# Optimization experiments

Measured on AMD Instinct MI355X. Metric: run time of the kernel, lower is better.

Reference implementation:

```python
import jax, jax.numpy as jnp
from jax import lax
import numpy as np

B, S, T = 512, 1024, 64  # batch, seq_len, tag_vocab_size


def setup_inputs() -> dict:
    key = jax.random.key(0)
    k1, k2, k3, k4 = jax.random.split(key, 4)
    tags = jax.random.randint(k1, (B, S), 0, T)
    # sequences sorted by length descending, as the original slicing scheme assumes
    lengths = jnp.sort(jax.random.randint(k2, (B,), 1, S + 1))[::-1]
    mask = jnp.arange(S)[None, :] < lengths[:, None]  # [B,S] bool
    emit_score = jax.random.normal(k3, (B, S, T), dtype=jnp.float32)
    transition = jax.random.normal(k4, (T, T), dtype=jnp.float32)
    return {"tags": tags, "mask": mask, "emit_score": emit_score, "transition": transition}


def reference(tags, mask, emit_score, transition):
    maskf = mask.astype(emit_score.dtype)
    # gold-path score: emission at gold tags + transition between consecutive gold tags
    score = jnp.take_along_axis(emit_score, tags[:, :, None], axis=2)[..., 0]  # [B,S]
    score = score.at[:, 1:].add(transition[tags[:, :-1], tags[:, 1:]])
    total_score = (score * maskf).sum(axis=1)  # [B]

    # forward algorithm (logsumexp-semiring scan over time)
    def step(d, inputs):
        emit_i, mask_i = inputs  # [B,T], [B]
        # log_sum[b, t_prev, t_cur] = d[b,t_prev] + transition[t_prev,t_cur] + emit_i[b,t_cur]
        cand = jax.nn.logsumexp(d[:, :, None] + transition[None, :, :] + emit_i[:, None, :], axis=1)
        d = jnp.where(mask_i[:, None], cand, d)  # finished sequences keep their alpha
        return d, None

    d0 = emit_score[:, 0]  # [B,T]
    emits_t = jnp.swapaxes(emit_score, 0, 1)[1:]  # [S-1,B,T]
    masks_t = mask.T[1:]  # [S-1,B]
    d, _ = lax.scan(step, d0, (emits_t, masks_t))
    log_z = jax.nn.logsumexp(d, axis=1)  # [B]
    return -(total_score - log_z)
```

## Files before the change

kernel.cpp:

```cpp
#include <hip/hip_runtime.h>
#include <stdint.h>

#define NB 512
#define SL 1024
#define NT 64

typedef float v4f __attribute__((ext_vector_type(4)));

__device__ __forceinline__ float wave_max6(float v) {
    #pragma unroll
    for (int off = 32; off >= 1; off >>= 1)
        v = fmaxf(v, __shfl_xor(v, off, 64));
    return v;
}
__device__ __forceinline__ float wave_sum_f(float v) {
    #pragma unroll
    for (int off = 32; off >= 1; off >>= 1)
        v += __shfl_xor(v, off, 64);
    return v;
}

__device__ __forceinline__ uint32_t bf16_rne(float x) {
    uint32_t u = __float_as_uint(x);
    return (u + 0x7fffu + ((u >> 16) & 1u)) >> 16;
}

__device__ __forceinline__ void dot2bf(float& acc, uint32_t a, uint32_t b) {
    asm("v_dot2_f32_bf16 %0, %1, %2, %0" : "+v"(acc) : "v"(a), "v"(b));
}

__global__ void __launch_bounds__(64) crf_fused_kernel(
    const int* __restrict__ tags, const void* __restrict__ mask,
    const float* __restrict__ emit, const float* __restrict__ trans,
    float* __restrict__ out)
{
    const int b = blockIdx.x;
    const int lane = threadIdx.x;
    const float* erow = emit + (size_t)b * SL * NT;
    const int* trow = tags + b * SL;

    const unsigned char* mb = (const unsigned char*)mask;
    const bool mask_is_i32 = ((mb[1] | mb[2] | mb[3]) == 0);

    float acc = 0.f; int cnt = 0;
    #pragma unroll
    for (int j = 0; j < 16; ++j) {
        const int i = lane + 64 * j;
        const int mk = mask_is_i32 ? (((const int*)mask)[(size_t)b * SL + i] != 0)
                                   : (mb[(size_t)b * SL + i] != 0);
        if (mk) {
            const int tg = trow[i];
            float val = erow[(size_t)i * NT + tg];
            if (i > 0) val += trans[trow[i - 1] * NT + tg];
            acc += val; cnt += 1;
        }
    }
    #pragma unroll
    for (int off = 32; off >= 1; off >>= 1) {
        acc += __shfl_xor(acc, off, 64);
        cnt += __shfl_xor(cnt, off, 64);
    }
    const float ts = acc;
    const int len = cnt;

    uint32_t Epk[NT / 2];
    #pragma unroll
    for (int m = 0; m < NT / 2; ++m) {
        uint32_t lo = bf16_rne(__expf(trans[(2 * m + 0) * NT + lane]));
        uint32_t hi = bf16_rne(__expf(trans[(2 * m + 1) * NT + lane]));
        Epk[m] = lo | (hi << 16);
    }

    __shared__ __align__(16) uint16_t vbuf16[NT];

    float d0 = erow[lane];
    float m0 = wave_max6(d0);
    float v = __expf(d0 - m0);
    float logacc = m0;

#define STEP(EX)                                                           \
    {                                                                      \
        vbuf16[lane] = (uint16_t)bf16_rne(v);                              \
        __builtin_amdgcn_wave_barrier();                                   \
        float a0 = 0.f, a1 = 0.f, a2 = 0.f, a3 = 0.f;                      \
        float a4 = 0.f, a5 = 0.f, a6 = 0.f, a7 = 0.f;                      \
        const uint4* vb = (const uint4*)vbuf16;                            \
        _Pragma("unroll")                                                  \
        for (int r = 0; r < 8; r += 2) {                                   \
            uint4 q0 = vb[r];                                              \
            uint4 q1 = vb[r + 1];                                          \
            dot2bf(a0, q0.x, Epk[4 * r + 0]);                              \
            dot2bf(a1, q0.y, Epk[4 * r + 1]);                              \
            dot2bf(a2, q0.z, Epk[4 * r + 2]);                              \
            dot2bf(a3, q0.w, Epk[4 * r + 3]);                              \
            dot2bf(a4, q1.x, Epk[4 * r + 4]);                              \
            dot2bf(a5, q1.y, Epk[4 * r + 5]);                              \
            dot2bf(a6, q1.z, Epk[4 * r + 6]);                              \
            dot2bf(a7, q1.w, Epk[4 * r + 7]);                              \
        }                                                                  \
        float h = ((a0 + a1) + (a2 + a3)) + ((a4 + a5) + (a6 + a7));       \
        v = h * (EX);                                                      \
    }

    const int nstep = len - 1;
    const int ngrp = nstep >> 2;
    int i = 1;

    v4f emq;
    if (ngrp > 0) {
        emq.x = erow[(i + 0) * NT + lane];
        emq.y = erow[(i + 1) * NT + lane];
        emq.z = erow[(i + 2) * NT + lane];
        emq.w = erow[(i + 3) * NT + lane];
    }
    for (int g = 0; g < ngrp; ++g) {
        float ex0 = __expf(emq.x), ex1 = __expf(emq.y);
        float ex2 = __expf(emq.z), ex3 = __expf(emq.w);
        const int ip = i + 4;
        if (g + 1 < ngrp) {
            emq.x = erow[(ip + 0) * NT + lane];
            emq.y = erow[(ip + 1) * NT + lane];
            emq.z = erow[(ip + 2) * NT + lane];
            emq.w = erow[(ip + 3) * NT + lane];
        }
        STEP(ex0)
        STEP(ex1)
        STEP(ex2)
        STEP(ex3)
        {
            uint32_t sb = __builtin_amdgcn_readfirstlane(__float_as_uint(v));
            int ex = (int)((sb >> 23) & 0xffu);
            v *= __uint_as_float((uint32_t)(254 - ex) << 23);
            logacc += (float)(ex - 127) * 0.69314718055994530942f;
        }
        i += 4;
    }
    for (; i < len; ++i) {
        float e = __expf(erow[i * NT + lane]);
        STEP(e)
    }
#undef STEP

    float sum = wave_sum_f(v);
    float log_z = logacc + __logf(sum);
    if (lane == 0) out[b] = -(ts - log_z);
}

extern "C" void kernel_launch(void* const* d_in, const int* in_sizes, int n_in,
                              void* d_out, int out_size, void* d_ws, size_t ws_size,
                              hipStream_t stream) {
    (void)in_sizes; (void)n_in; (void)out_size; (void)d_ws; (void)ws_size;
    const int*   tags  = (const int*)d_in[0];
    const void*  mask  = d_in[1];
    const float* emit  = (const float*)d_in[2];
    const float* trans = (const float*)d_in[3];
    float* out = (float*)d_out;

    crf_fused_kernel<<<dim3(NB), dim3(64), 0, stream>>>(tags, mask, emit, trans, out);
}
```

Measured before the change: 385.8 us.

## Batch 16 sequences per wave with MFMA scan over precomputed bf16 exp-emissions

```diff
diff --git a/kernel.cpp b/kernel.cpp
--- a/kernel.cpp
+++ b/kernel.cpp
@@ -4,32 +4,222 @@
 #define NB 512
 #define SL 1024
 #define NT 64
-
-typedef float v4f __attribute__((ext_vector_type(4)));
-
-__device__ __forceinline__ float wave_max6(float v) {
-    #pragma unroll
-    for (int off = 32; off >= 1; off >>= 1)
-        v = fmaxf(v, __shfl_xor(v, off, 64));
-    return v;
-}
-__device__ __forceinline__ float wave_sum_f(float v) {
-    #pragma unroll
-    for (int off = 32; off >= 1; off >>= 1)
-        v += __shfl_xor(v, off, 64);
-    return v;
-}
+#define NG 32
+#define GR 16
+
+typedef float f32x4 __attribute__((ext_vector_type(4)));
+typedef float v2f  __attribute__((ext_vector_type(2)));
+typedef short s16x8 __attribute__((ext_vector_type(8)));
 
 __device__ __forceinline__ uint32_t bf16_rne(float x) {
     uint32_t u = __float_as_uint(x);
     return (u + 0x7fffu + ((u >> 16) & 1u)) >> 16;
 }
+__device__ __forceinline__ uint32_t pack_bf16_trunc(float lo, float hi) {
+    return __builtin_amdgcn_perm(__float_as_uint(hi), __float_as_uint(lo), 0x07060302u);
+}
+__device__ __forceinline__ int t_of(int c, int q, int e) {
+    return 16 * (((c << 1) | (e >> 2))) + 4 * q + (e & 3);
+}
+
+__device__ __forceinline__ float wave_max6(float v) {
+    #pragma unroll
+    for (int off = 32; off >= 1; off >>= 1) v = fmaxf(v, __shfl_xor(v, off, 64));
+    return v;
+}
+__device__ __forceinline__ float wave_sum_f(float v) {
+    #pragma unroll
+    for (int off = 32; off >= 1; off >>= 1) v += __shfl_xor(v, off, 64);
+    return v;
+}
+
+__global__ void __launch_bounds__(256) exp_permute_kernel(
+    const float* __restrict__ emit, uint32_t* __restrict__ em4)
+{
+    __shared__ float tile[GR][16 * NT];
+    const int g = blockIdx.x >> 6;
+    const int i0 = (blockIdx.x & 63) << 4;
+    const int tid = threadIdx.x;
+
+    #pragma unroll 4
+    for (int bb = 0; bb < GR; ++bb) {
+        const float4* src = (const float4*)(emit + ((size_t)(GR * g + bb) * SL + i0) * NT);
+        ((float4*)tile[bb])[tid] = src[tid];
+    }
+    __syncthreads();
+
+    const int i_loc = tid >> 4;
+    const int lane0 = (tid & 15) << 2;
+    uint4 outq[8];
+    uint32_t* ov = (uint32_t*)outq;
+    #pragma unroll
+    for (int li = 0; li < 4; ++li) {
+        const int lane = lane0 + li, q = lane >> 4, r = lane & 15;
+        #pragma unroll
+        for (int d = 0; d < 8; ++d) {
+            const int c = d >> 2, dd = d & 3;
+            const int t0 = t_of(c, q, 2 * dd + 0);
+            const int t1 = t_of(c, q, 2 * dd + 1);
+            const float f0 = __expf(tile[r][i_loc * NT + t0]);
+            const float f1 = __expf(tile[r][i_loc * NT + t1]);
+            ov[li * 8 + d] = bf16_rne(f0) | (bf16_rne(f1) << 16);
+        }
+    }
+    uint4* dst = (uint4*)(em4 + (((size_t)(g * SL + i0 + i_loc) * 64) + lane0) * 8);
+    #pragma unroll
+    for (int k = 0; k < 8; ++k) dst[k] = outq[k];
+}
+
+template<bool DOREN>
+__device__ __forceinline__ void scan_step(
+    const s16x8 (&A)[4][2], uint4& B0, uint4& B1,
+    uint4 em0, uint4 em1, int i, int len, float& logacc)
+{
+    union U { uint4 u; s16x8 h; };
+    U b0; b0.u = B0; U b1; b1.u = B1;
+    const f32x4 z = {0.f, 0.f, 0.f, 0.f};
+    f32x4 acc[4];
+    #pragma unroll
+    for (int mi = 0; mi < 4; ++mi) {
+        f32x4 t = __builtin_amdgcn_mfma_f32_16x16x32_bf16(A[mi][0], b0.h, z, 0, 0, 0);
+        acc[mi]  = __builtin_amdgcn_mfma_f32_16x16x32_bf16(A[mi][1], b1.h, t, 0, 0, 0);
+    }
+    const uint32_t ed[8] = {em0.x, em0.y, em0.z, em0.w, em1.x, em1.y, em1.z, em1.w};
+    v2f p[8];
+    #pragma unroll
+    for (int s = 0; s < 8; ++s) {
+        const int c = s >> 2, d = s & 3;
+        const int mi = (c << 1) | (d >> 1);
+        const int rb = (d & 1) * 2;
+        const float elo = __uint_as_float(ed[s] << 16);
+        const float ehi = __uint_as_float(ed[s] & 0xffff0000u);
+        p[s].x = acc[mi][rb] * elo;
+        p[s].y = acc[mi][rb + 1] * ehi;
+    }
+    const bool alive = (i < len);
+    if (DOREN) {
+        float mx = 0.f;
+        #pragma unroll
+        for (int s = 0; s < 8; ++s) mx = fmaxf(mx, fmaxf(p[s].x, p[s].y));
+        mx = fmaxf(mx, __shfl_xor(mx, 16, 64));
+        mx = fmaxf(mx, __shfl_xor(mx, 32, 64));
+        const int ex = (int)((__float_as_uint(mx) >> 23) & 0xffu);
+        float sc = __uint_as_float((uint32_t)(254 - ex) << 23);
+        sc = alive ? sc : 1.0f;
+        logacc += alive ? (float)(ex - 127) * 0.69314718055994530942f : 0.0f;
+        #pragma unroll
+        for (int s = 0; s < 8; ++s) { p[s].x *= sc; p[s].y *= sc; }
+    }
+    uint32_t nd[8];
+    #pragma unroll
+    for (int s = 0; s < 8; ++s) nd[s] = pack_bf16_trunc(p[s].x, p[s].y);
+    B0.x = alive ? nd[0] : B0.x;  B0.y = alive ? nd[1] : B0.y;
+    B0.z = alive ? nd[2] : B0.z;  B0.w = alive ? nd[3] : B0.w;
+    B1.x = alive ? nd[4] : B1.x;  B1.y = alive ? nd[5] : B1.y;
+    B1.z = alive ? nd[6] : B1.z;  B1.w = alive ? nd[7] : B1.w;
+}
+
+__global__ void __launch_bounds__(64) crf_scan16_kernel(
+    const int* __restrict__ tags, const void* __restrict__ mask,
+    const float* __restrict__ emit, const float* __restrict__ trans,
+    const uint32_t* __restrict__ em4, float* __restrict__ out)
+{
+    const int g = blockIdx.x;
+    const int lane = threadIdx.x;
+    const int q = lane >> 4, r = lane & 15;
+    const int b = GR * g + r;
+
+    const unsigned char* mb = (const unsigned char*)mask;
+    const bool mask_is_i32 = ((mb[1] | mb[2] | mb[3]) == 0);
+    const int* trow = tags + (size_t)b * SL;
+    float acc = 0.f; int cnt = 0;
+    for (int ii = 0; ii < 256; ++ii) {
+        const int i = q * 256 + ii;
+        const int mk = mask_is_i32 ? (((const int*)mask)[(size_t)b * SL + i] != 0)
+                                   : (mb[(size_t)b * SL + i] != 0);
+        if (mk) {
+            const int tg = trow[i];
+            float val = emit[((size_t)b * SL + i) * NT + tg];
+            if (i > 0) val += trans[trow[i - 1] * NT + tg];
+            acc += val; cnt += 1;
+        }
+    }
+    acc += __shfl_xor(acc, 16, 64); acc += __shfl_xor(acc, 32, 64);
+    cnt += __shfl_xor(cnt, 16, 64); cnt += __shfl_xor(cnt, 32, 64);
+    const float ts = acc;
+    const int len = cnt;
+    int mx = len;
+    #pragma unroll
+    for (int off = 1; off <= 8; off <<= 1) mx = max(mx, __shfl_xor(mx, off, 64));
+    const int nstep = __builtin_amdgcn_readfirstlane(mx) - 1;
+
+    s16x8 A[4][2];
+    #pragma unroll
+    for (int mi = 0; mi < 4; ++mi)
+        #pragma unroll
+        for (int c = 0; c < 2; ++c)
+            #pragma unroll
+            for (int e = 0; e < 8; ++e) {
+                const int p = t_of(c, q, e);
+                A[mi][c][e] = (short)bf16_rne(__expf(trans[p * NT + (16 * mi + r)]));
+            }
+
+    const uint4* em_base = (const uint4*)em4 + (size_t)g * SL * 128 + (size_t)lane * 2;
+    uint4 B0 = em_base[0], B1 = em_base[1];
+    float logacc = 0.f;
+
+    int i = 1;
+    uint4 bufA[4][2], bufB[4][2];
+    #pragma unroll
+    for (int s = 0; s < 4; ++s) {
+        int sa = min(i + s, SL - 1), sb = min(i + 4 + s, SL - 1);
+        const uint4* pA = em_base + (size_t)sa * 128;
+        const uint4* pB = em_base + (size_t)sb * 128;
+        bufA[s][0] = pA[0]; bufA[s][1] = pA[1];
+        bufB[s][0] = pB[0]; bufB[s][1] = pB[1];
+    }
+    const int nsuper = nstep >> 3;
+    for (int sb = 0; sb < nsuper; ++sb) {
+        scan_step<false>(A, B0, B1, bufA[0][0], bufA[0][1], i + 0, len, logacc);
+        scan_step<false>(A, B0, B1, bufA[1][0], bufA[1][1], i + 1, len, logacc);
+        scan_step<false>(A, B0, B1, bufA[2][0], bufA[2][1], i + 2, len, logacc);
+        scan_step<true >(A, B0, B1, bufA[3][0], bufA[3][1], i + 3, len, logacc);
+        #pragma unroll
+        for (int s = 0; s < 4; ++s) {
+            const uint4* pp = em_base + (size_t)min(i + 8 + s, SL - 1) * 128;
+            bufA[s][0] = pp[0]; bufA[s][1] = pp[1];
+        }
+        scan_step<false>(A, B0, B1, bufB[0][0], bufB[0][1], i + 4, len, logacc);
+        scan_step<false>(A, B0, B1, bufB[1][0], bufB[1][1], i + 5, len, logacc);
+        scan_step<false>(A, B0, B1, bufB[2][0], bufB[2][1], i + 6, len, logacc);
+        scan_step<true >(A, B0, B1, bufB[3][0], bufB[3][1], i + 7, len, logacc);
+        #pragma unroll
+        for (int s = 0; s < 4; ++s) {
+            const uint4* pp = em_base + (size_t)min(i + 12 + s, SL - 1) * 128;
+            bufB[s][0] = pp[0]; bufB[s][1] = pp[1];
+        }
+        i += 8;
+    }
+    for (; i <= nstep; ++i) {
+        const uint4* pp = em_base + (size_t)i * 128;
+        scan_step<true>(A, B0, B1, pp[0], pp[1], i, len, logacc);
+    }
+
+    const uint32_t fd[8] = {B0.x, B0.y, B0.z, B0.w, B1.x, B1.y, B1.z, B1.w};
+    float sum = 0.f;
+    #pragma unroll
+    for (int s = 0; s < 8; ++s)
+        sum += __uint_as_float(fd[s] << 16) + __uint_as_float(fd[s] & 0xffff0000u);
+    sum += __shfl_xor(sum, 16, 64);
+    sum += __shfl_xor(sum, 32, 64);
+    const float log_z = logacc + __logf(sum);
+    if (lane < GR) out[(size_t)g * GR + lane] = -(ts - log_z);
+}
 
 __device__ __forceinline__ void dot2bf(float& acc, uint32_t a, uint32_t b) {
     asm("v_dot2_f32_bf16 %0, %1, %2, %0" : "+v"(acc) : "v"(a), "v"(b));
 }
-
-__global__ void __launch_bounds__(64) crf_fused_kernel(
+__global__ void __launch_bounds__(64) crf_fallback_kernel(
     const int* __restrict__ tags, const void* __restrict__ mask,
     const float* __restrict__ emit, const float* __restrict__ trans,
     float* __restrict__ out)
@@ -37,11 +227,9 @@
     const int b = blockIdx.x;
     const int lane = threadIdx.x;
     const float* erow = emit + (size_t)b * SL * NT;
-    const int* trow = tags + b * SL;
-
+    const int* trow = tags + (size_t)b * SL;
     const unsigned char* mb = (const unsigned char*)mask;
     const bool mask_is_i32 = ((mb[1] | mb[2] | mb[3]) == 0);
-
     float acc = 0.f; int cnt = 0;
     #pragma unroll
     for (int j = 0; j < 16; ++j) {
@@ -60,9 +248,7 @@
         acc += __shfl_xor(acc, off, 64);
         cnt += __shfl_xor(cnt, off, 64);
     }
-    const float ts = acc;
-    const int len = cnt;
-
+    const float ts = acc; const int len = cnt;
     uint32_t Epk[NT / 2];
     #pragma unroll
     for (int m = 0; m < NT / 2; ++m) {
@@ -70,77 +256,53 @@
         uint32_t hi = bf16_rne(__expf(trans[(2 * m + 1) * NT + lane]));
         Epk[m] = lo | (hi << 16);
     }
-
     __shared__ __align__(16) uint16_t vbuf16[NT];
-
     float d0 = erow[lane];
     float m0 = wave_max6(d0);
     float v = __expf(d0 - m0);
     float logacc = m0;
-
-#define STEP(EX)                                                           \
+#define FSTEP(EX)                                                          \
     {                                                                      \
         vbuf16[lane] = (uint16_t)bf16_rne(v);                              \
         __builtin_amdgcn_wave_barrier();                                   \
-        float a0 = 0.f, a1 = 0.f, a2 = 0.f, a3 = 0.f;                      \
-        float a4 = 0.f, a5 = 0.f, a6 = 0.f, a7 = 0.f;                      \
+        float a0=0.f,a1=0.f,a2=0.f,a3=0.f,a4=0.f,a5=0.f,a6=0.f,a7=0.f;     \
         const uint4* vb = (const uint4*)vbuf16;                            \
         _Pragma("unroll")                                                  \
-        for (int r = 0; r < 8; r += 2) {                                   \
-            uint4 q0 = vb[r];                                              \
-            uint4 q1 = vb[r + 1];                                          \
-            dot2bf(a0, q0.x, Epk[4 * r + 0]);                              \
-            dot2bf(a1, q0.y, Epk[4 * r + 1]);                              \
-            dot2bf(a2, q0.z, Epk[4 * r + 2]);                              \
-            dot2bf(a3, q0.w, Epk[4 * r + 3]);                              \
-            dot2bf(a4, q1.x, Epk[4 * r + 4]);                              \
-            dot2bf(a5, q1.y, Epk[4 * r + 5]);                              \
-            dot2bf(a6, q1.z, Epk[4 * r + 6]);                              \
-            dot2bf(a7, q1.w, Epk[4 * r + 7]);                              \
+        for (int rr = 0; rr < 8; rr += 2) {                                \
+            uint4 q0 = vb[rr]; uint4 q1 = vb[rr + 1];                      \
+            dot2bf(a0, q0.x, Epk[4*rr+0]); dot2bf(a1, q0.y, Epk[4*rr+1]);  \
+            dot2bf(a2, q0.z, Epk[4*rr+2]); dot2bf(a3, q0.w, Epk[4*rr+3]);  \
+            dot2bf(a4, q1.x, Epk[4*rr+4]); dot2bf(a5, q1.y, Epk[4*rr+5]);  \
+            dot2bf(a6, q1.z, Epk[4*rr+6]); dot2bf(a7, q1.w, Epk[4*rr+7]);  \
         }                                                                  \
-        float h = ((a0 + a1) + (a2 + a3)) + ((a4 + a5) + (a6 + a7));       \
-        v = h * (EX);                                                      \
-    }
-
-    const int nstep = len - 1;
-    const int ngrp = nstep >> 2;
+        v = (((a0+a1)+(a2+a3))+((a4+a5)+(a6+a7))) * (EX);                  \
+    }
+    const int nstep = len - 1, ngrp = nstep >> 2;
     int i = 1;
-
-    v4f emq;
+    float4 emq;
     if (ngrp > 0) {
-        emq.x = erow[(i + 0) * NT + lane];
-        emq.y = erow[(i + 1) * NT + lane];
-        emq.z = erow[(i + 2) * NT + lane];
-        emq.w = erow[(i + 3) * NT + lane];
-    }
-    for (int g = 0; g < ngrp; ++g) {
+        emq.x = erow[(i+0)*NT+lane]; emq.y = erow[(i+1)*NT+lane];
+        emq.z = erow[(i+2)*NT+lane]; emq.w = erow[(i+3)*NT+lane];
+    }
+    for (int gg = 0; gg < ngrp; ++gg) {
         float ex0 = __expf(emq.x), ex1 = __expf(emq.y);
         float ex2 = __expf(emq.z), ex3 = __expf(emq.w);
         const int ip = i + 4;
-        if (g + 1 < ngrp) {
-            emq.x = erow[(ip + 0) * NT + lane];
-            emq.y = erow[(ip + 1) * NT + lane];
-            emq.z = erow[(ip + 2) * NT + lane];
-            emq.w = erow[(ip + 3) * NT + lane];
-        }
-        STEP(ex0)
-        STEP(ex1)
-        STEP(ex2)
-        STEP(ex3)
+        if (gg + 1 < ngrp) {
+            emq.x = erow[(ip+0)*NT+lane]; emq.y = erow[(ip+1)*NT+lane];
+            emq.z = erow[(ip+2)*NT+lane]; emq.w = erow[(ip+3)*NT+lane];
+        }
+        FSTEP(ex0) FSTEP(ex1) FSTEP(ex2) FSTEP(ex3)
         {
-            uint32_t sb = __builtin_amdgcn_readfirstlane(__float_as_uint(v));
-            int ex = (int)((sb >> 23) & 0xffu);
+            uint32_t sb2 = __builtin_amdgcn_readfirstlane(__float_as_uint(v));
+            int ex = (int)((sb2 >> 23) & 0xffu);
             v *= __uint_as_float((uint32_t)(254 - ex) << 23);
             logacc += (float)(ex - 127) * 0.69314718055994530942f;
         }
         i += 4;
     }
-    for (; i < len; ++i) {
-        float e = __expf(erow[i * NT + lane]);
-        STEP(e)
-    }
-#undef STEP
-
+    for (; i < len; ++i) { float e = __expf(erow[i * NT + lane]); FSTEP(e) }
+#undef FSTEP
     float sum = wave_sum_f(v);
     float log_z = logacc + __logf(sum);
     if (lane == 0) out[b] = -(ts - log_z);
@@ -149,12 +311,19 @@
 extern "C" void kernel_launch(void* const* d_in, const int* in_sizes, int n_in,
                               void* d_out, int out_size, void* d_ws, size_t ws_size,
                               hipStream_t stream) {
-    (void)in_sizes; (void)n_in; (void)out_size; (void)d_ws; (void)ws_size;
+    (void)in_sizes; (void)n_in; (void)out_size;
     const int*   tags  = (const int*)d_in[0];
     const void*  mask  = d_in[1];
     const float* emit  = (const float*)d_in[2];
     const float* trans = (const float*)d_in[3];
     float* out = (float*)d_out;
 
-    crf_fused_kernel<<<dim3(NB), dim3(64), 0, stream>>>(tags, mask, emit, trans, out);
-}
+    const size_t EM4_BYTES = (size_t)NB * SL * NT * 2;
+    if (ws_size >= EM4_BYTES) {
+        exp_permute_kernel<<<dim3(NG * 64), dim3(256), 0, stream>>>(emit, (uint32_t*)d_ws);
+        crf_scan16_kernel<<<dim3(NG), dim3(64), 0, stream>>>(
+            tags, mask, emit, trans, (const uint32_t*)d_ws, out);
+    } else {
+        crf_fallback_kernel<<<dim3(NB), dim3(64), 0, stream>>>(tags, mask, emit, trans, out);
+    }
+}
```

After: 715.3 us. 85.4% more time.
